# Optimization experiments

Measured on AMD Instinct MI355X. Metric: run time of the kernel, lower is better.

Reference implementation:

```python
import jax, jax.numpy as jnp
import numpy as np


def setup_inputs() -> dict:
    key = jax.random.key(0)
    B, M, S, H, D = 1, 32768, 512, 8, 64
    ks = jax.random.split(key, 5)
    f = lambda k, shape: jax.random.normal(k, shape, dtype=jnp.float32)
    return {
        "mem_keys": f(ks[0], (B, M, H, D)),
        "mem_vals": f(ks[1], (B, M, H, D)),
        "keys": f(ks[2], (B, S, H, D)),
        "values": f(ks[3], (B, S, H, D)),
        "queries": f(ks[4], (B, S, H, D)),
        "start_of_sequence": jnp.zeros((B,), dtype=jnp.bool_),
        "write_index": 0,
    }


def reference(mem_keys, mem_vals, keys, values, queries, start_of_sequence, write_index):
    """DenseKVMemory: start_segment (clear), read (joint attention), end_segment (scatter write).

    Returns (y, new_mem_keys, new_mem_vals, new_write_index).
    """
    B, S, H, D = keys.shape
    M = mem_keys.shape[1]
    dtype = mem_keys.dtype

    # --- start_segment: clear memory at document boundaries ---
    keep = jnp.logical_not(start_of_sequence).astype(dtype).reshape(B, 1, 1, 1)
    mem_keys_c = mem_keys * keep
    mem_vals_c = mem_vals * keep

    # --- read: joint attention over [memory (no mask), segment (causal mask)] ---
    scale = float(D) ** -0.5  # default 1/sqrt(head_size) when attention_scale_factor is None
    q = queries * jnp.asarray(scale, dtype)
    mem_logits = jnp.einsum('bqhd,bkhd->bhqk', q, mem_keys_c)  # [B,H,S,M]
    seg_logits = jnp.einsum('bqhd,bkhd->bhqk', q, keys)        # [B,H,S,S]

    # kq_pos = key_pos - (query_pos + queries_offset); queries_offset = 0 at segment start.
    # causal_mask True (kq_pos < 0): key strictly before query -> allowed.
    kq_pos = jnp.arange(S)[None, :] - jnp.arange(S)[:, None]
    causal_mask = kq_pos < 0  # [S,S]
    neg_inf = jnp.asarray(jnp.finfo(dtype).min, dtype)
    seg_logits = jnp.where(causal_mask[None, None, :, :], seg_logits, neg_inf)

    all_logits = jnp.concatenate([mem_logits, seg_logits], axis=-1)  # [B,H,S,M+S]
    weights = jax.nn.softmax(all_logits, axis=-1)
    all_vals = jnp.concatenate([mem_vals_c, values], axis=1)         # [B,M+S,H,D]
    y = jnp.einsum('bhqk,bkhd->bqhd', weights, all_vals)             # [B,S,H,D]

    # --- end_segment: scatter-write segment KV into the ring buffer ---
    wi = jnp.asarray(write_index, jnp.int32)
    new_mem_keys = jax.lax.dynamic_update_slice_in_dim(mem_keys_c, keys, wi, axis=1)
    new_mem_vals = jax.lax.dynamic_update_slice_in_dim(mem_vals_c, values, wi, axis=1)
    new_write_index = (wi + S) % M
    return (y, new_mem_keys, new_mem_vals, new_write_index)
```

## Files before the change

kernel.cpp:

```cpp
#include <hip/hip_runtime.h>
#include <hip/hip_bf16.h>

typedef __bf16 bf16x8 __attribute__((ext_vector_type(8)));
typedef __bf16 bf16x4 __attribute__((ext_vector_type(4)));
typedef __bf16 bf16x2 __attribute__((ext_vector_type(2)));
typedef float f32x4 __attribute__((ext_vector_type(4)));

#define M_MEM 32768
#define S_SEG 512
#define H_ 8
#define D_ 64
#define NKEY 33280
#define NTILES 520
#define LOG2E 1.44269504088896340736f
#define CMAX (14.0f * LOG2E)

#define Y_OFF 0
#define NK_OFF 262144
#define WI_OFF (262144 + 2 * 16777216)

__global__ __launch_bounds__(256, 3) void fused_attn(
    const float* __restrict__ memk, const float* __restrict__ memv,
    const float* __restrict__ keys, const float* __restrict__ vals,
    const float* __restrict__ qry, const unsigned char* __restrict__ sos,
    const int* __restrict__ wip, float* __restrict__ out,
    float* __restrict__ opart, float* __restrict__ lst, int NC) {
  const int bid = blockIdx.x;
  const int tid = threadIdx.x;
  const int c = bid >> 5;
  const int qp = (bid >> 3) & 3;
  const int h = bid & 7;
  const int w = tid >> 6;
  const int lane = tid & 63;
  const int L = lane & 15;
  const int quad = lane >> 4;
  const float keep = sos[0] ? 0.0f : 1.0f;

  int wi_raw = wip[0];
  int wi = wi_raw < 0 ? 0 : (wi_raw > M_MEM - S_SEG ? M_MEM - S_SEG : wi_raw);
  if (bid == 0 && tid == 0) {
    int nwi = (int)(((long long)wi_raw + S_SEG) % M_MEM);
    if (nwi < 0) nwi += M_MEM;
    out[WI_OFF] = (float)nwi;
  }

  __shared__ __align__(16) __bf16 Ks[64 * 72];
  __shared__ __align__(16) __bf16 Vt[64 * 72];
  __shared__ __align__(16) __bf16 Pt[4][16 * 64];

  const int qA = qp * 128 + w * 16 + L;
  const int qB = qA + 64;

  bf16x8 qfA[2], qfB[2];
  {
    const float qs = 0.125f * LOG2E;
    const float* qpA = qry + ((size_t)qA * H_ + h) * D_;
    const float* qpB = qry + ((size_t)qB * H_ + h) * D_;
#pragma unroll
    for (int kb = 0; kb < 2; ++kb) {
      const int d = kb * 32 + quad * 8;
      float4 a0 = *(const float4*)(qpA + d);
      float4 a1 = *(const float4*)(qpA + d + 4);
      float4 b0 = *(const float4*)(qpB + d);
      float4 b1 = *(const float4*)(qpB + d + 4);
      bf16x8 fa, fb;
      fa[0] = (__bf16)(a0.x * qs); fa[1] = (__bf16)(a0.y * qs);
      fa[2] = (__bf16)(a0.z * qs); fa[3] = (__bf16)(a0.w * qs);
      fa[4] = (__bf16)(a1.x * qs); fa[5] = (__bf16)(a1.y * qs);
      fa[6] = (__bf16)(a1.z * qs); fa[7] = (__bf16)(a1.w * qs);
      fb[0] = (__bf16)(b0.x * qs); fb[1] = (__bf16)(b0.y * qs);
      fb[2] = (__bf16)(b0.z * qs); fb[3] = (__bf16)(b0.w * qs);
      fb[4] = (__bf16)(b1.x * qs); fb[5] = (__bf16)(b1.y * qs);
      fb[6] = (__bf16)(b1.z * qs); fb[7] = (__bf16)(b1.w * qs);
      qfA[kb] = fa; qfB[kb] = fb;
    }
  }

  f32x4 accA[4], accB[4];
#pragma unroll
  for (int g = 0; g < 4; ++g) {
    accA[g] = (f32x4){0.f, 0.f, 0.f, 0.f};
    accB[g] = (f32x4){0.f, 0.f, 0.f, 0.f};
  }
  float lA = 0.f, lB = 0.f;

  const int tile_start = (NTILES * c) / NC;
  const int tile_end = (NTILES * (c + 1)) / NC;
  const int nt = tile_end - tile_start;

  const int kk = tid >> 2;
  const int d0 = (tid & 3) * 16;
  const int vp2 = tid & 31;
  const int dvb = (tid >> 5) * 8;

  float4 kreg[4], vreg[4];
  float mult;
  auto issue = [&](int t) {
    const int tb = (tile_start + t) * 64;
    const float *kb_, *vb_;
    if (tb < M_MEM) {
      kb_ = memk + (size_t)tb * 512 + h * 64;
      vb_ = memv + (size_t)tb * 512 + h * 64;
      mult = keep;
    } else {
      kb_ = keys + (size_t)(tb - M_MEM) * 512 + h * 64;
      vb_ = vals + (size_t)(tb - M_MEM) * 512 + h * 64;
      mult = 1.0f;
    }
    const float* ks = kb_ + (size_t)kk * 512 + d0;
#pragma unroll
    for (int i = 0; i < 4; ++i) kreg[i] = *(const float4*)(ks + i * 4);
    const float* vs = vb_ + (size_t)(2 * vp2) * 512 + dvb;
    vreg[0] = *(const float4*)(vs);
    vreg[1] = *(const float4*)(vs + 4);
    vreg[2] = *(const float4*)(vs + 512);
    vreg[3] = *(const float4*)(vs + 516);
  };

  issue(0);
  for (int t = 0; t < nt; ++t) {
    const int tb = (tile_start + t) * 64;
    const float mu = mult;
    if (mu != 0.0f) {
      bf16x8 lo, hi;
      lo[0] = (__bf16)kreg[0].x; lo[1] = (__bf16)kreg[0].y;
      lo[2] = (__bf16)kreg[0].z; lo[3] = (__bf16)kreg[0].w;
      lo[4] = (__bf16)kreg[1].x; lo[5] = (__bf16)kreg[1].y;
      lo[6] = (__bf16)kreg[1].z; lo[7] = (__bf16)kreg[1].w;
      hi[0] = (__bf16)kreg[2].x; hi[1] = (__bf16)kreg[2].y;
      hi[2] = (__bf16)kreg[2].z; hi[3] = (__bf16)kreg[2].w;
      hi[4] = (__bf16)kreg[3].x; hi[5] = (__bf16)kreg[3].y;
      hi[6] = (__bf16)kreg[3].z; hi[7] = (__bf16)kreg[3].w;
      *(bf16x8*)&Ks[kk * 72 + d0] = lo;
      *(bf16x8*)&Ks[kk * 72 + d0 + 8] = hi;
      const int col = (2 * vp2 + dvb) & 63;
      float a0[8] = {vreg[0].x, vreg[0].y, vreg[0].z, vreg[0].w,
                     vreg[1].x, vreg[1].y, vreg[1].z, vreg[1].w};
      float a1[8] = {vreg[2].x, vreg[2].y, vreg[2].z, vreg[2].w,
                     vreg[3].x, vreg[3].y, vreg[3].z, vreg[3].w};
#pragma unroll
      for (int i = 0; i < 8; ++i) {
        bf16x2 pr;
        pr[0] = (__bf16)a0[i];
        pr[1] = (__bf16)a1[i];
        *(bf16x2*)&Vt[(dvb + i) * 72 + col] = pr;
      }
    } else {
      bf16x8 zk = {};
      *(bf16x8*)&Ks[kk * 72 + d0] = zk;
      *(bf16x8*)&Ks[kk * 72 + d0 + 8] = zk;
      const int col = (2 * vp2 + dvb) & 63;
      bf16x2 z2 = {};
#pragma unroll
      for (int i = 0; i < 8; ++i) *(bf16x2*)&Vt[(dvb + i) * 72 + col] = z2;
    }
    if ((((unsigned)(tb >> 6)) & 3u) == (unsigned)qp) {
      int krow = (tb < M_MEM) ? tb + kk : wi + (tb - M_MEM) + kk;
      bool kskip = (tb < M_MEM) && (krow >= wi && krow < wi + S_SEG);
      if (!kskip) {
        float* dK = out + NK_OFF + (size_t)krow * 512 + h * 64 + d0;
#pragma unroll
        for (int i = 0; i < 4; ++i) {
          float4 vv = kreg[i];
          vv.x *= mu; vv.y *= mu; vv.z *= mu; vv.w *= mu;
          *(float4*)(dK + i * 4) = vv;
        }
      }
      int r0 = (tb < M_MEM) ? tb + 2 * vp2 : wi + (tb - M_MEM) + 2 * vp2;
#pragma unroll
      for (int pk2 = 0; pk2 < 2; ++pk2) {
        int vrow = r0 + pk2;
        bool vskip = (tb < M_MEM) && (vrow >= wi && vrow < wi + S_SEG);
        if (!vskip) {
          float* dV = out + NK_OFF + 16777216 + (size_t)vrow * 512 + h * 64 + dvb;
          float4 u0 = vreg[pk2 * 2], u1 = vreg[pk2 * 2 + 1];
          u0.x *= mu; u0.y *= mu; u0.z *= mu; u0.w *= mu;
          *(float4*)(dV) = u0;
          *(float4*)(dV + 4) = u1;
        }
      }
    }
    __syncthreads();
    if (t + 1 < nt) issue(t + 1);

    f32x4 sgA[4], sgB[4];
#pragma unroll
    for (int g = 0; g < 4; ++g) {
      bf16x8 klo = *(bf16x8*)&Ks[(g * 16 + L) * 72 + quad * 8];
      bf16x8 khi = *(bf16x8*)&Ks[(g * 16 + L) * 72 + 32 + quad * 8];
      f32x4 zA = (f32x4){0.f, 0.f, 0.f, 0.f};
      f32x4 zB = (f32x4){0.f, 0.f, 0.f, 0.f};
      zA = __builtin_amdgcn_mfma_f32_16x16x32_bf16(klo, qfA[0], zA, 0, 0, 0);
      zB = __builtin_amdgcn_mfma_f32_16x16x32_bf16(klo, qfB[0], zB, 0, 0, 0);
      sgA[g] = __builtin_amdgcn_mfma_f32_16x16x32_bf16(khi, qfA[1], zA, 0, 0, 0);
      sgB[g] = __builtin_amdgcn_mfma_f32_16x16x32_bf16(khi, qfB[1], zB, 0, 0, 0);
    }

    const int prot = 8 * (L & 7);
    const bool segt = (tb >= M_MEM);
#pragma unroll
    for (int g = 0; g < 4; ++g) {
      bf16x4 pk;
#pragma unroll
      for (int r = 0; r < 4; ++r) {
        float p = __builtin_amdgcn_exp2f(sgA[g][r] - CMAX);
        if (segt) {
          const int kseg = tb - M_MEM + g * 16 + quad * 4 + r;
          p = (kseg >= qA) ? 0.f : p;
        }
        lA += p;
        pk[r] = (__bf16)p;
      }
      *(bf16x4*)&Pt[w][L * 64 + ((g * 16 + quad * 4 + prot) & 63)] = pk;
    }
    bf16x8 pbA0 = *(bf16x8*)&Pt[w][L * 64 + ((quad * 8 + prot) & 63)];
    bf16x8 pbA1 = *(bf16x8*)&Pt[w][L * 64 + ((32 + quad * 8 + prot) & 63)];

    bf16x4 pkB[4];
#pragma unroll
    for (int g = 0; g < 4; ++g) {
      bf16x4 pk;
#pragma unroll
      for (int r = 0; r < 4; ++r) {
        float p = __builtin_amdgcn_exp2f(sgB[g][r] - CMAX);
        if (segt) {
          const int kseg = tb - M_MEM + g * 16 + quad * 4 + r;
          p = (kseg >= qB) ? 0.f : p;
        }
        lB += p;
        pk[r] = (__bf16)p;
      }
      pkB[g] = pk;
    }
    asm volatile("s_waitcnt lgkmcnt(0)" ::: "memory");
#pragma unroll
    for (int g = 0; g < 4; ++g)
      *(bf16x4*)&Pt[w][L * 64 + ((g * 16 + quad * 4 + prot) & 63)] = pkB[g];
    bf16x8 pbB0 = *(bf16x8*)&Pt[w][L * 64 + ((quad * 8 + prot) & 63)];
    bf16x8 pbB1 = *(bf16x8*)&Pt[w][L * 64 + ((32 + quad * 8 + prot) & 63)];

#pragma unroll
    for (int g = 0; g < 4; ++g) {
      const int vrot = g * 16 + 8 * (L >> 3);
      bf16x8 v0 = *(bf16x8*)&Vt[(g * 16 + L) * 72 + ((quad * 8 + vrot) & 63)];
      bf16x8 v1 = *(bf16x8*)&Vt[(g * 16 + L) * 72 + ((32 + quad * 8 + vrot) & 63)];
      accA[g] = __builtin_amdgcn_mfma_f32_16x16x32_bf16(v0, pbA0, accA[g], 0, 0, 0);
      accA[g] = __builtin_amdgcn_mfma_f32_16x16x32_bf16(v1, pbA1, accA[g], 0, 0, 0);
      accB[g] = __builtin_amdgcn_mfma_f32_16x16x32_bf16(v0, pbB0, accB[g], 0, 0, 0);
      accB[g] = __builtin_amdgcn_mfma_f32_16x16x32_bf16(v1, pbB1, accB[g], 0, 0, 0);
    }
    __syncthreads();
  }

  lA += __shfl_xor(lA, 16);
  lA += __shfl_xor(lA, 32);
  lB += __shfl_xor(lB, 16);
  lB += __shfl_xor(lB, 32);
  const size_t rowA = (size_t)h * S_SEG + qA;
  const size_t rowB = (size_t)h * S_SEG + qB;
#pragma unroll
  for (int g = 0; g < 4; ++g) {
    *(f32x4*)&opart[(rowA * NC + c) * 64 + g * 16 + quad * 4] = accA[g];
    *(f32x4*)&opart[(rowB * NC + c) * 64 + g * 16 + quad * 4] = accB[g];
  }
  if (quad == 0) {
    lst[rowA * NC + c] = lA;
    lst[rowB * NC + c] = lB;
  }
}

__global__ __launch_bounds__(256) void combine(
    const float* __restrict__ opart, const float* __restrict__ lst,
    float* __restrict__ y, int NC) {
  const int idx = blockIdx.x * 256 + threadIdx.x;
  const int d = idx & 63;
  const int h = (idx >> 6) & 7;
  const int q = idx >> 9;
  const size_t row = (size_t)h * S_SEG + q;
  float num = 0.f, den = 0.f;
  for (int c = 0; c < NC; ++c) {
    num += opart[(row * NC + c) * 64 + d];
    den += lst[row * NC + c];
  }
  y[idx] = num / den;
}

extern "C" void kernel_launch(void* const* d_in, const int* in_sizes, int n_in,
                              void* d_out, int out_size, void* d_ws, size_t ws_size,
                              hipStream_t stream) {
  const float* memk = (const float*)d_in[0];
  const float* memv = (const float*)d_in[1];
  const float* keys = (const float*)d_in[2];
  const float* vals = (const float*)d_in[3];
  const float* qry  = (const float*)d_in[4];
  const unsigned char* sos = (const unsigned char*)d_in[5];
  const int* wip = (const int*)d_in[6];
  float* out = (float*)d_out;

  static const int cand[] = {40, 32, 24, 20, 16, 10, 8, 5, 4, 2, 1};
  int NC = 1;
  for (int i = 0; i < 11; ++i) {
    size_t need = (size_t)cand[i] *
        ((size_t)H_ * S_SEG * D_ * 4 + (size_t)H_ * S_SEG * 4);
    if (need <= ws_size) { NC = cand[i]; break; }
  }

  float* opart = (float*)d_ws;
  float* lstp = opart + (size_t)H_ * S_SEG * NC * D_;

  fused_attn<<<NC * 32, 256, 0, stream>>>(
      memk, memv, keys, vals, qry, sos, wip, out, opart, lstp, NC);

  combine<<<1024, 256, 0, stream>>>(opart, lstp, out + Y_OFF, NC);
}
```

Before: 326.4 us.

## Double-buffer K/V tiles in LDS and feed P to MFMA directly from registers

K and V tiles now live in two LDS buffers, so staging the next tile overlaps computing the current one and each iteration needs only one barrier instead of two. The P tile no longer round-trips through LDS: the QK^T output is consumed in registers by 16x16x16 bf16 MFMAs, whose input layout matches the accumulator layout. V loading and transposition were reorganised to write bf16x4, and the PV section raises wave priority with s_setprio. Occupancy is raised to 4 waves per SIMD and NC=24 is dropped. The risks are the doubled LDS use, register pressure at the higher occupancy, and twice as many smaller MFMAs in the PV step.

```diff
diff --git a/kernel.cpp b/kernel.cpp
--- a/kernel.cpp
+++ b/kernel.cpp
@@ -5,6 +5,7 @@
 typedef __bf16 bf16x4 __attribute__((ext_vector_type(4)));
 typedef __bf16 bf16x2 __attribute__((ext_vector_type(2)));
 typedef float f32x4 __attribute__((ext_vector_type(4)));
+typedef short short4_ __attribute__((ext_vector_type(4)));
 
 #define M_MEM 32768
 #define S_SEG 512
@@ -19,7 +20,21 @@
 #define NK_OFF 262144
 #define WI_OFF (262144 + 2 * 16777216)
 
-__global__ __launch_bounds__(256, 3) void fused_attn(
+static __device__ inline f32x4 mfma16(bf16x4 a, bf16x4 b, f32x4 c) {
+#if __has_builtin(__builtin_amdgcn_mfma_f32_16x16x16_bf16)
+  return __builtin_amdgcn_mfma_f32_16x16x16_bf16(a, b, c, 0, 0, 0);
+#elif __has_builtin(__builtin_amdgcn_mfma_f32_16x16x16bf16_1k)
+  short4_ as = __builtin_bit_cast(short4_, a);
+  short4_ bs = __builtin_bit_cast(short4_, b);
+  return __builtin_amdgcn_mfma_f32_16x16x16bf16_1k(as, bs, c, 0, 0, 0);
+#else
+  asm volatile("v_mfma_f32_16x16x16_bf16 %0, %1, %2, %0"
+               : "+v"(c) : "v"(a), "v"(b));
+  return c;
+#endif
+}
+
+__global__ __launch_bounds__(256, 4) void fused_attn(
     const float* __restrict__ memk, const float* __restrict__ memv,
     const float* __restrict__ keys, const float* __restrict__ vals,
     const float* __restrict__ qry, const unsigned char* __restrict__ sos,
@@ -44,9 +59,8 @@
     out[WI_OFF] = (float)nwi;
   }
 
-  __shared__ __align__(16) __bf16 Ks[64 * 72];
-  __shared__ __align__(16) __bf16 Vt[64 * 72];
-  __shared__ __align__(16) __bf16 Pt[4][16 * 64];
+  __shared__ __align__(16) __bf16 Ks[2][64 * 72];
+  __shared__ __align__(16) __bf16 Vt[2][64 * 72];
 
   const int qA = qp * 128 + w * 16 + L;
   const int qB = qA + 64;
@@ -90,8 +104,9 @@
 
   const int kk = tid >> 2;
   const int d0 = (tid & 3) * 16;
-  const int vp2 = tid & 31;
-  const int dvb = (tid >> 5) * 8;
+  const int dv4 = (tid & 15) * 4;
+  const int key4 = (tid >> 4) * 4;
+  const int vrot = (dv4 >> 3) * 8;
 
   float4 kreg[4], vreg[4];
   float mult;
@@ -110,15 +125,12 @@
     const float* ks = kb_ + (size_t)kk * 512 + d0;
 #pragma unroll
     for (int i = 0; i < 4; ++i) kreg[i] = *(const float4*)(ks + i * 4);
-    const float* vs = vb_ + (size_t)(2 * vp2) * 512 + dvb;
-    vreg[0] = *(const float4*)(vs);
-    vreg[1] = *(const float4*)(vs + 4);
-    vreg[2] = *(const float4*)(vs + 512);
-    vreg[3] = *(const float4*)(vs + 516);
+    const float* vs = vb_ + (size_t)key4 * 512 + dv4;
+#pragma unroll
+    for (int i = 0; i < 4; ++i) vreg[i] = *(const float4*)(vs + i * 512);
   };
 
-  issue(0);
-  for (int t = 0; t < nt; ++t) {
+  auto stage = [&](int pbuf, int t) {
     const int tb = (tile_start + t) * 64;
     const float mu = mult;
     if (mu != 0.0f) {
@@ -131,28 +143,24 @@
       hi[2] = (__bf16)kreg[2].z; hi[3] = (__bf16)kreg[2].w;
       hi[4] = (__bf16)kreg[3].x; hi[5] = (__bf16)kreg[3].y;
       hi[6] = (__bf16)kreg[3].z; hi[7] = (__bf16)kreg[3].w;
-      *(bf16x8*)&Ks[kk * 72 + d0] = lo;
-      *(bf16x8*)&Ks[kk * 72 + d0 + 8] = hi;
-      const int col = (2 * vp2 + dvb) & 63;
-      float a0[8] = {vreg[0].x, vreg[0].y, vreg[0].z, vreg[0].w,
-                     vreg[1].x, vreg[1].y, vreg[1].z, vreg[1].w};
-      float a1[8] = {vreg[2].x, vreg[2].y, vreg[2].z, vreg[2].w,
-                     vreg[3].x, vreg[3].y, vreg[3].z, vreg[3].w};
-#pragma unroll
-      for (int i = 0; i < 8; ++i) {
-        bf16x2 pr;
-        pr[0] = (__bf16)a0[i];
-        pr[1] = (__bf16)a1[i];
-        *(bf16x2*)&Vt[(dvb + i) * 72 + col] = pr;
+      *(bf16x8*)&Ks[pbuf][kk * 72 + d0] = lo;
+      *(bf16x8*)&Ks[pbuf][kk * 72 + d0 + 8] = hi;
+      const int col = (key4 + vrot) & 63;
+#pragma unroll
+      for (int i = 0; i < 4; ++i) {
+        bf16x4 pk;
+        pk[0] = (__bf16)vreg[0][i]; pk[1] = (__bf16)vreg[1][i];
+        pk[2] = (__bf16)vreg[2][i]; pk[3] = (__bf16)vreg[3][i];
+        *(bf16x4*)&Vt[pbuf][(dv4 + i) * 72 + col] = pk;
       }
     } else {
       bf16x8 zk = {};
-      *(bf16x8*)&Ks[kk * 72 + d0] = zk;
-      *(bf16x8*)&Ks[kk * 72 + d0 + 8] = zk;
-      const int col = (2 * vp2 + dvb) & 63;
-      bf16x2 z2 = {};
-#pragma unroll
-      for (int i = 0; i < 8; ++i) *(bf16x2*)&Vt[(dvb + i) * 72 + col] = z2;
+      *(bf16x8*)&Ks[pbuf][kk * 72 + d0] = zk;
+      *(bf16x8*)&Ks[pbuf][kk * 72 + d0 + 8] = zk;
+      const int col = (key4 + vrot) & 63;
+      bf16x4 z4 = {};
+#pragma unroll
+      for (int i = 0; i < 4; ++i) *(bf16x4*)&Vt[pbuf][(dv4 + i) * 72 + col] = z4;
     }
     if ((((unsigned)(tb >> 6)) & 3u) == (unsigned)qp) {
       int krow = (tb < M_MEM) ? tb + kk : wi + (tb - M_MEM) + kk;
@@ -166,90 +174,78 @@
           *(float4*)(dK + i * 4) = vv;
         }
       }
-      int r0 = (tb < M_MEM) ? tb + 2 * vp2 : wi + (tb - M_MEM) + 2 * vp2;
-#pragma unroll
-      for (int pk2 = 0; pk2 < 2; ++pk2) {
-        int vrow = r0 + pk2;
+#pragma unroll
+      for (int i = 0; i < 4; ++i) {
+        int vrow = (tb < M_MEM) ? tb + key4 + i : wi + (tb - M_MEM) + key4 + i;
         bool vskip = (tb < M_MEM) && (vrow >= wi && vrow < wi + S_SEG);
         if (!vskip) {
-          float* dV = out + NK_OFF + 16777216 + (size_t)vrow * 512 + h * 64 + dvb;
-          float4 u0 = vreg[pk2 * 2], u1 = vreg[pk2 * 2 + 1];
-          u0.x *= mu; u0.y *= mu; u0.z *= mu; u0.w *= mu;
-          *(float4*)(dV) = u0;
-          *(float4*)(dV + 4) = u1;
+          float* dV = out + NK_OFF + 16777216 + (size_t)vrow * 512 + h * 64 + dv4;
+          float4 u = vreg[i];
+          u.x *= mu; u.y *= mu; u.z *= mu; u.w *= mu;
+          *(float4*)(dV) = u;
         }
       }
     }
-    __syncthreads();
-    if (t + 1 < nt) issue(t + 1);
-
-    f32x4 sgA[4], sgB[4];
+  };
+
+  auto compute = [&](int t, int pbuf) {
+    const int tb = (tile_start + t) * 64;
+    const bool segt = (tb >= M_MEM);
+    const __bf16* KsB = &Ks[pbuf][0];
+    const __bf16* VtB = &Vt[pbuf][0];
+    bf16x4 pA[4], pB4[4];
 #pragma unroll
     for (int g = 0; g < 4; ++g) {
-      bf16x8 klo = *(bf16x8*)&Ks[(g * 16 + L) * 72 + quad * 8];
-      bf16x8 khi = *(bf16x8*)&Ks[(g * 16 + L) * 72 + 32 + quad * 8];
+      bf16x8 klo = *(const bf16x8*)&KsB[(g * 16 + L) * 72 + quad * 8];
+      bf16x8 khi = *(const bf16x8*)&KsB[(g * 16 + L) * 72 + 32 + quad * 8];
       f32x4 zA = (f32x4){0.f, 0.f, 0.f, 0.f};
       f32x4 zB = (f32x4){0.f, 0.f, 0.f, 0.f};
       zA = __builtin_amdgcn_mfma_f32_16x16x32_bf16(klo, qfA[0], zA, 0, 0, 0);
       zB = __builtin_amdgcn_mfma_f32_16x16x32_bf16(klo, qfB[0], zB, 0, 0, 0);
-      sgA[g] = __builtin_amdgcn_mfma_f32_16x16x32_bf16(khi, qfA[1], zA, 0, 0, 0);
-      sgB[g] = __builtin_amdgcn_mfma_f32_16x16x32_bf16(khi, qfB[1], zB, 0, 0, 0);
-    }
-
-    const int prot = 8 * (L & 7);
-    const bool segt = (tb >= M_MEM);
-#pragma unroll
-    for (int g = 0; g < 4; ++g) {
-      bf16x4 pk;
+      zA = __builtin_amdgcn_mfma_f32_16x16x32_bf16(khi, qfA[1], zA, 0, 0, 0);
+      zB = __builtin_amdgcn_mfma_f32_16x16x32_bf16(khi, qfB[1], zB, 0, 0, 0);
 #pragma unroll
       for (int r = 0; r < 4; ++r) {
-        float p = __builtin_amdgcn_exp2f(sgA[g][r] - CMAX);
+        float pa = __builtin_amdgcn_exp2f(zA[r] - CMAX);
+        float pb = __builtin_amdgcn_exp2f(zB[r] - CMAX);
         if (segt) {
           const int kseg = tb - M_MEM + g * 16 + quad * 4 + r;
-          p = (kseg >= qA) ? 0.f : p;
+          pa = (kseg >= qA) ? 0.f : pa;
+          pb = (kseg >= qB) ? 0.f : pb;
         }
-        lA += p;
-        pk[r] = (__bf16)p;
-      }
-      *(bf16x4*)&Pt[w][L * 64 + ((g * 16 + quad * 4 + prot) & 63)] = pk;
-    }
-    bf16x8 pbA0 = *(bf16x8*)&Pt[w][L * 64 + ((quad * 8 + prot) & 63)];
-    bf16x8 pbA1 = *(bf16x8*)&Pt[w][L * 64 + ((32 + quad * 8 + prot) & 63)];
-
-    bf16x4 pkB[4];
-#pragma unroll
-    for (int g = 0; g < 4; ++g) {
-      bf16x4 pk;
-#pragma unroll
-      for (int r = 0; r < 4; ++r) {
-        float p = __builtin_amdgcn_exp2f(sgB[g][r] - CMAX);
-        if (segt) {
-          const int kseg = tb - M_MEM + g * 16 + quad * 4 + r;
-          p = (kseg >= qB) ? 0.f : p;
-        }
-        lB += p;
-        pk[r] = (__bf16)p;
-      }
-      pkB[g] = pk;
-    }
-    asm volatile("s_waitcnt lgkmcnt(0)" ::: "memory");
-#pragma unroll
-    for (int g = 0; g < 4; ++g)
-      *(bf16x4*)&Pt[w][L * 64 + ((g * 16 + quad * 4 + prot) & 63)] = pkB[g];
-    bf16x8 pbB0 = *(bf16x8*)&Pt[w][L * 64 + ((quad * 8 + prot) & 63)];
-    bf16x8 pbB1 = *(bf16x8*)&Pt[w][L * 64 + ((32 + quad * 8 + prot) & 63)];
-
-#pragma unroll
-    for (int g = 0; g < 4; ++g) {
-      const int vrot = g * 16 + 8 * (L >> 3);
-      bf16x8 v0 = *(bf16x8*)&Vt[(g * 16 + L) * 72 + ((quad * 8 + vrot) & 63)];
-      bf16x8 v1 = *(bf16x8*)&Vt[(g * 16 + L) * 72 + ((32 + quad * 8 + vrot) & 63)];
-      accA[g] = __builtin_amdgcn_mfma_f32_16x16x32_bf16(v0, pbA0, accA[g], 0, 0, 0);
-      accA[g] = __builtin_amdgcn_mfma_f32_16x16x32_bf16(v1, pbA1, accA[g], 0, 0, 0);
-      accB[g] = __builtin_amdgcn_mfma_f32_16x16x32_bf16(v0, pbB0, accB[g], 0, 0, 0);
-      accB[g] = __builtin_amdgcn_mfma_f32_16x16x32_bf16(v1, pbB1, accB[g], 0, 0, 0);
-    }
-    __syncthreads();
+        lA += pa; lB += pb;
+        pA[g][r] = (__bf16)pa;
+        pB4[g][r] = (__bf16)pb;
+      }
+    }
+    __builtin_amdgcn_s_setprio(1);
+#pragma unroll
+    for (int dg = 0; dg < 4; ++dg) {
+      const int rowb = (dg * 16 + L) * 72;
+      const int rot = dg * 16 + 8 * (L >> 3);
+#pragma unroll
+      for (int g = 0; g < 4; ++g) {
+        bf16x4 vf = *(const bf16x4*)&VtB[rowb + ((g * 16 + quad * 4 + rot) & 63)];
+        accA[dg] = mfma16(vf, pA[g], accA[dg]);
+        accB[dg] = mfma16(vf, pB4[g], accB[dg]);
+      }
+    }
+    __builtin_amdgcn_s_setprio(0);
+  };
+
+  issue(0);
+  stage(0, 0);
+  if (nt > 1) issue(1);
+  __syncthreads();
+  int pb = 0;
+  for (int t = 0; t < nt; ++t) {
+    compute(t, pb);
+    if (t + 1 < nt) {
+      stage(pb ^ 1, t + 1);
+      if (t + 2 < nt) issue(t + 2);
+      __syncthreads();
+      pb ^= 1;
+    }
   }
 
   lA += __shfl_xor(lA, 16);
@@ -297,9 +293,9 @@
   const int* wip = (const int*)d_in[6];
   float* out = (float*)d_out;
 
-  static const int cand[] = {40, 32, 24, 20, 16, 10, 8, 5, 4, 2, 1};
+  static const int cand[] = {40, 32, 20, 16, 10, 8, 5, 4, 2, 1};
   int NC = 1;
-  for (int i = 0; i < 11; ++i) {
+  for (int i = 0; i < 10; ++i) {
     size_t need = (size_t)cand[i] *
         ((size_t)H_ * S_SEG * D_ * 4 + (size_t)H_ * S_SEG * 4);
     if (need <= ws_size) { NC = cand[i]; break; }
```

New measurement: 562.6 us. 72.3% more time.
